# Performance work log

Hardware: AMD Instinct MI355X
Metric: run time of the kernel (lower is better)

Reference implementation:

```python
import jax, jax.numpy as jnp
import numpy as np

NUM_HEADS = 16
ROPE_SEGMENTS = (1024, 512)  # remainder of the sequence is left un-roped
ROPE_THETA = 10000.0
EPS = 1e-6


def _rmsnorm(t, w):
    # t: [B,H,N,D]; norm over last dim in fp32, then scale
    tf = t.astype(jnp.float32)
    n = tf * jax.lax.rsqrt(jnp.mean(tf * tf, axis=-1, keepdims=True) + EPS)
    return n.astype(t.dtype) * w


def _rope(t):
    # t: [B,H,S,D]; positions restart at 0 for each call (segment-local RoPE)
    S, D = t.shape[-2], t.shape[-1]
    inv_freq = 1.0 / (ROPE_THETA ** (jnp.arange(0, D, 2, dtype=jnp.float32) / D))  # [D/2]
    ang = jnp.arange(S, dtype=jnp.float32)[:, None] * inv_freq[None, :]            # [S,D/2]
    cos, sin = jnp.cos(ang), jnp.sin(ang)
    t1, t2 = t[..., : D // 2], t[..., D // 2 :]
    return jnp.concatenate([t1 * cos - t2 * sin, t2 * cos + t1 * sin], axis=-1).astype(t.dtype)


def _segmented_rope(t, N):
    parts, start = [], 0
    for seg in ROPE_SEGMENTS:
        parts.append(_rope(t[:, :, start : start + seg, :]))
        start += seg
    if start < N:
        parts.append(t[:, :, start:, :])
    return jnp.concatenate(parts, axis=2)


def setup_inputs() -> dict:
    key = jax.random.key(0)
    ks = jax.random.split(key, 5)
    B, N, C = 2, 2048, 1024
    D = C // NUM_HEADS
    s = 1.0 / np.sqrt(C)
    return {
        "x": jax.random.normal(ks[0], (B, N, C), jnp.float32),
        "qkv_w": jax.random.normal(ks[1], (3 * C, C), jnp.float32) * s,
        "qkv_b": jax.random.normal(ks[2], (3 * C,), jnp.float32) * 0.02,
        "qn_w": jnp.ones((D,), jnp.float32),
        "kn_w": jnp.ones((D,), jnp.float32),
        "proj_w": jax.random.normal(ks[3], (C, C), jnp.float32) * s,
        "proj_b": jax.random.normal(ks[4], (C,), jnp.float32) * 0.02,
    }


def reference(x, qkv_w, qkv_b, qn_w, kn_w, proj_w, proj_b):
    B, N, C = x.shape
    H = NUM_HEADS
    D = C // H
    qkv = (x @ qkv_w.T + qkv_b).reshape(B, N, 3, H, D)
    qkv = jnp.transpose(qkv, (2, 0, 3, 1, 4))  # [3,B,H,N,D]
    q, k, v = qkv[0], qkv[1], qkv[2]
    q = _rmsnorm(q, qn_w)
    k = _rmsnorm(k, kn_w)
    q = _segmented_rope(q, N)
    k = _segmented_rope(k, N)
    scale = 1.0 / np.sqrt(D)  # SDPA default scale
    scores = jnp.einsum("bhqd,bhkd->bhqk", q, k) * scale
    attn = jax.nn.softmax(scores, axis=-1)
    out = jnp.einsum("bhqk,bhkd->bhqd", attn, v)           # [B,H,N,D]
    out = jnp.transpose(out, (0, 2, 1, 3)).reshape(B, N, C)
    return out @ proj_w.T + proj_b
```

## Files before the change

kernel.cpp:

```cpp
#include <hip/hip_runtime.h>

typedef __attribute__((ext_vector_type(8))) short short8;
typedef __attribute__((ext_vector_type(4))) float f32x4;
typedef __attribute__((ext_vector_type(16))) float f32x16;

__device__ __forceinline__ float bf2f(unsigned short u) {
    union { unsigned int i; float f; } c; c.i = ((unsigned int)u) << 16; return c.f;
}
__device__ __forceinline__ unsigned short f2bf(float f) {
    union { float f; unsigned int i; } c; c.f = f;
    unsigned int u = c.i;
    return (unsigned short)((u + 0x7fffu + ((u >> 16) & 1u)) >> 16);
}

__device__ __forceinline__ void glds16(const void* g, void* l) {
    __builtin_amdgcn_global_load_lds(
        (const __attribute__((address_space(1))) unsigned int*)g,
        (__attribute__((address_space(3))) unsigned int*)l, 16, 0, 0);
}

union i4s8 { int4 i; short8 s; };

__global__ __launch_bounds__(256) void prep(
    const float* __restrict__ x, const float* __restrict__ qkv_w,
    const float* __restrict__ proj_w,
    const float* __restrict__ qn_w, const float* __restrict__ kn_w,
    unsigned short* __restrict__ xb, unsigned short* __restrict__ qwb,
    unsigned short* __restrict__ pwb, float* __restrict__ mb2)
{
    const int b = blockIdx.x, tid = threadIdx.x;
    const float* src; unsigned short* dst; int i;
    if (b < 4096)      { src = x;      dst = xb;  i = b * 256 + tid; }
    else if (b < 7168) { src = qkv_w;  dst = qwb; i = (b - 4096) * 256 + tid; }
    else if (b < 8192) { src = proj_w; dst = pwb; i = (b - 7168) * 256 + tid; }
    else {
        if (tid < 64) {
            float a = fabsf(qn_w[tid]), bb = fabsf(kn_w[tid]);
#pragma unroll
            for (int off = 32; off; off >>= 1) {
                a = fmaxf(a, __shfl_xor(a, off));
                bb = fmaxf(bb, __shfl_xor(bb, off));
            }
            if (tid == 0) *mb2 = 8.0f * a * bb * 1.4426950408889634f;
        }
        return;
    }
    float4 v = ((const float4*)src)[i];
    ushort4 o;
    o.x = f2bf(v.x); o.y = f2bf(v.y); o.z = f2bf(v.z); o.w = f2bf(v.w);
    ((ushort4*)dst)[i] = o;
}

__global__ __launch_bounds__(256) void gemm_qkv(
    const unsigned short* __restrict__ A,
    const unsigned short* __restrict__ W,
    const float* __restrict__ bias,
    const float* __restrict__ qn_w, const float* __restrict__ kn_w,
    unsigned short* __restrict__ qb, unsigned short* __restrict__ kb,
    unsigned short* __restrict__ vt)
{
    __shared__ unsigned short pool[128 * 136];
    const int tid = threadIdx.x;
    const int w = tid >> 6, l = tid & 63, quad = l >> 4, low = l & 15;
    const int m0 = blockIdx.y * 128, n0 = blockIdx.x * 128;
    const int wm = w >> 1, wn = w & 1;
    const int K = 1024;

    f32x4 acc[4][4];
#pragma unroll
    for (int i = 0; i < 4; i++)
#pragma unroll
        for (int j = 0; j < 4; j++) acc[i][j] = (f32x4){0.f, 0.f, 0.f, 0.f};

    const int r1 = tid >> 2, p1 = tid & 3;
    const int c1 = p1 ^ ((r1 >> 1) & 3);
    const int r2 = r1 + 64;
    const int c2 = p1 ^ ((r2 >> 1) & 3);
    const unsigned short* ga1 = A + (size_t)(m0 + r1) * K + c1 * 8;
    const unsigned short* ga2 = A + (size_t)(m0 + r2) * K + c2 * 8;
    const unsigned short* gw1 = W + (size_t)(n0 + r1) * K + c1 * 8;
    const unsigned short* gw2 = W + (size_t)(n0 + r2) * K + c2 * 8;
    char* lA = (char*)pool + (w << 10);
    char* lW = (char*)pool + 8192 + (w << 10);

    for (int k0 = 0; k0 < K; k0 += 32) {
        __syncthreads();
        glds16(ga1 + k0, lA);
        glds16(ga2 + k0, lA + 4096);
        glds16(gw1 + k0, lW);
        glds16(gw2 + k0, lW + 4096);
        __syncthreads();
        short8 af[4], wf[4];
#pragma unroll
        for (int i = 0; i < 4; i++) {
            const int ra = wm * 64 + i * 16 + low;
            af[i] = *(const short8*)&pool[ra * 32 + (quad ^ ((ra >> 1) & 3)) * 8];
            const int rw = wn * 64 + i * 16 + low;
            wf[i] = *(const short8*)&pool[4096 + rw * 32 + (quad ^ ((rw >> 1) & 3)) * 8];
        }
#pragma unroll
        for (int i = 0; i < 4; i++)
#pragma unroll
            for (int j = 0; j < 4; j++)
                acc[i][j] = __builtin_amdgcn_mfma_f32_16x16x32_bf16(
                    af[i], wf[j], acc[i][j], 0, 0, 0);
    }

    const int colbase = n0 + wn * 64;
    const int t3 = n0 >> 10;
    const int hh = (colbase & 1023) >> 6;

    if (t3 == 2) {
        __syncthreads();
#pragma unroll
        for (int i = 0; i < 4; i++)
#pragma unroll
            for (int j = 0; j < 4; j++) {
                const int c = wn * 64 + j * 16 + low;
                const float bv = bias[n0 + c];
#pragma unroll
                for (int reg = 0; reg < 4; reg++) {
                    const int r = wm * 64 + i * 16 + quad * 4 + reg;
                    pool[c * 136 + r] = f2bf(acc[i][j][reg] + bv);
                }
            }
        __syncthreads();
        const int b_ = m0 >> 11, nbase = m0 & 2047;
        const int rch = (tid & 15) * 8;
#pragma unroll
        for (int p = 0; p < 8; p++) {
            const int c = (tid >> 4) + p * 16;
            const int gc = n0 + c;
            const int h2 = (gc & 1023) >> 6, d = gc & 63;
            const short8 vv = *(const short8*)&pool[c * 136 + rch];
            *(short8*)(vt + ((size_t)((b_ * 16 + h2) * 64 + d)) * 2048 + nbase + rch) = vv;
        }
        return;
    }

    const float* nw = (t3 == 0) ? qn_w : kn_w;
    float wv4[4];
#pragma unroll
    for (int j = 0; j < 4; j++) wv4[j] = nw[j * 16 + low];
    const float c0 = -2.0f * 13.287712379549449f / 64.0f;
    const float invA = exp2f(c0 * (float)low);
    const float invB = exp2f(c0 * (float)(16 + low));
    unsigned short* dqk = (t3 == 0) ? qb : kb;

#pragma unroll
    for (int i = 0; i < 4; i++) {
#pragma unroll
        for (int reg = 0; reg < 4; reg++) {
            const int gm = m0 + wm * 64 + i * 16 + quad * 4 + reg;
            const int b_ = gm >> 11, npos = gm & 2047;
            float v[4];
#pragma unroll
            for (int j = 0; j < 4; j++)
                v[j] = acc[i][j][reg] + bias[colbase + j * 16 + low];
            float ss = v[0]*v[0] + v[1]*v[1] + v[2]*v[2] + v[3]*v[3];
            ss += __shfl_xor(ss, 1); ss += __shfl_xor(ss, 2);
            ss += __shfl_xor(ss, 4); ss += __shfl_xor(ss, 8);
            const float r = rsqrtf(ss * (1.0f / 64.0f) + 1e-6f);
            float nv[4];
#pragma unroll
            for (int j = 0; j < 4; j++) nv[j] = v[j] * r * wv4[j];
            float o0, o1, o2, o3;
            if (npos < 1536) {
                const float p = (float)((npos < 1024) ? npos : (npos - 1024));
                float sA, cA, sB, cB;
                __sincosf(p * invA, &sA, &cA);
                __sincosf(p * invB, &sB, &cB);
                o0 = nv[0] * cA - nv[2] * sA;
                o1 = nv[1] * cB - nv[3] * sB;
                o2 = nv[2] * cA + nv[0] * sA;
                o3 = nv[3] * cB + nv[1] * sB;
            } else { o0 = nv[0]; o1 = nv[1]; o2 = nv[2]; o3 = nv[3]; }
            unsigned short* drow =
                dqk + ((size_t)(b_ * 16 + hh) * 2048 + npos) * 64 + low;
            drow[0]  = f2bf(o0);
            drow[16] = f2bf(o1);
            drow[32] = f2bf(o2);
            drow[48] = f2bf(o3);
        }
    }
}

__global__ __launch_bounds__(256, 4) void flash_mfma(
    const unsigned short* __restrict__ qg, const unsigned short* __restrict__ kg,
    const unsigned short* __restrict__ vg, unsigned short* __restrict__ po,
    float* __restrict__ pl, const float* __restrict__ mb2p)
{
    __shared__ unsigned short Ks[128 * 64];
    __shared__ unsigned short Vs[64 * 128];

    const int tid = threadIdx.x;
    const int w = tid >> 6, lane = tid & 63, h5 = lane >> 5, l5 = lane & 31;
    const int bh = blockIdx.y, q0 = blockIdx.x * 128, half = blockIdx.z;
    const float MB2 = *mb2p;
    const float SCL = 0.125f * 1.4426950408889634f;

    short8 qf[4];
    {
        const unsigned short* qrow = qg + ((size_t)bh * 2048 + q0 + w * 32 + l5) * 64;
#pragma unroll
        for (int ks = 0; ks < 4; ks++)
            qf[ks] = *(const short8*)(qrow + ks * 16 + h5 * 8);
    }

    f32x16 o0, o1, ls;
#pragma unroll
    for (int i = 0; i < 16; i++) { o0[i] = 0.f; o1[i] = 0.f; ls[i] = 0.f; }
    i4s8 ones; ones.i = make_int4(0x3F803F80, 0x3F803F80, 0x3F803F80, 0x3F803F80);

    const int krr = tid >> 3, kc = (tid & 7) ^ (krr & 7);
    const unsigned short* gk = kg + ((size_t)bh * 2048 + krr) * 64 + kc * 8;
    const int vrr = tid >> 4, vc = (tid & 15) ^ (vrr & 15);
    const unsigned short* gv = vg + ((size_t)bh * 64 + vrr) * 2048 + vc * 8;
    char* lK = (char*)Ks + (w << 10);
    char* lV = (char*)Vs + (w << 10);
    const int kbase = half * 1024;

    for (int kt = 0; kt < 8; kt++) {
        const size_t ko = (size_t)(kbase + kt * 128);
        __syncthreads();
        glds16(gk + ko * 64,         lK);
        glds16(gk + ko * 64 + 2048,  lK + 4096);
        glds16(gk + ko * 64 + 4096,  lK + 8192);
        glds16(gk + ko * 64 + 6144,  lK + 12288);
        glds16(gv + ko,              lV);
        glds16(gv + ko + 32768,      lV + 4096);
        glds16(gv + ko + 65536,      lV + 8192);
        glds16(gv + ko + 98304,      lV + 12288);
        __syncthreads();

#pragma unroll
        for (int kbk = 0; kbk < 4; kbk++) {
            f32x16 s;
#pragma unroll
            for (int i = 0; i < 16; i++) s[i] = 0.f;
            const int krow = kbk * 32 + l5;
#pragma unroll
            for (int ks = 0; ks < 4; ks++) {
                const int ch = (h5 + 2 * ks) ^ (krow & 7);
                const short8 kf = *(const short8*)&Ks[krow * 64 + ch * 8];
                s = __builtin_amdgcn_mfma_f32_32x32x16_bf16(kf, qf[ks], s, 0, 0, 0);
            }
            unsigned int dw[8], pdw[8];
#pragma unroll
            for (int r = 0; r < 8; r++) {
                union { float f; unsigned int u; } a, b;
                a.f = exp2f(fmaf(s[2 * r],     SCL, -MB2));
                b.f = exp2f(fmaf(s[2 * r + 1], SCL, -MB2));
                dw[r] = __builtin_amdgcn_perm(b.u, a.u, 0x07060302u);
            }
#pragma unroll
            for (int r = 0; r < 8; r++) pdw[r] = __shfl_xor((int)dw[r], 32);
            i4s8 f0, f1;
            f0.i.x = h5 ? pdw[2] : dw[0];
            f0.i.y = h5 ? pdw[3] : dw[1];
            f0.i.z = h5 ? dw[2]  : pdw[0];
            f0.i.w = h5 ? dw[3]  : pdw[1];
            f1.i.x = h5 ? pdw[6] : dw[4];
            f1.i.y = h5 ? pdw[7] : dw[5];
            f1.i.z = h5 ? dw[6]  : pdw[4];
            f1.i.w = h5 ? dw[7]  : pdw[5];

            ls = __builtin_amdgcn_mfma_f32_32x32x16_bf16(f0.s, ones.s, ls, 0, 0, 0);
            ls = __builtin_amdgcn_mfma_f32_32x32x16_bf16(f1.s, ones.s, ls, 0, 0, 0);

#pragma unroll
            for (int nb = 0; nb < 2; nb++) {
                const int vrow = nb * 32 + l5;
                const int chb = kbk * 4 + h5;
                const short8 vfa = *(const short8*)&Vs[vrow * 128 + ((chb    ) ^ (vrow & 15)) * 8];
                const short8 vfb = *(const short8*)&Vs[vrow * 128 + ((chb + 2) ^ (vrow & 15)) * 8];
                f32x16& oo = nb ? o1 : o0;
                oo = __builtin_amdgcn_mfma_f32_32x32x16_bf16(f0.s, vfa, oo, 0, 0, 0);
                oo = __builtin_amdgcn_mfma_f32_32x32x16_bf16(f1.s, vfb, oo, 0, 0, 0);
            }
        }
    }

    unsigned short* pob = po + ((size_t)(half * 32 + bh)) * 2048 * 64;
    float* plb = pl + ((size_t)(half * 32 + bh)) * 2048;
#pragma unroll
    for (int r = 0; r < 16; r++) {
        const int qrow = q0 + w * 32 + (r & 3) + 8 * (r >> 2) + 4 * h5;
        pob[(size_t)qrow * 64 + l5]      = f2bf(o0[r]);
        pob[(size_t)qrow * 64 + 32 + l5] = f2bf(o1[r]);
        if (l5 == 0) plb[qrow] = ls[r];
    }
}

__global__ __launch_bounds__(256) void combine(
    const unsigned short* __restrict__ po, const float* __restrict__ pl,
    unsigned short* __restrict__ ao)
{
    const int g = blockIdx.x * 256 + threadIdx.x;
    const int row = g >> 3;
    const int c8 = (g & 7) * 8;
    const int bh = row >> 11, n = row & 2047;
    const float inv = 1.0f / (pl[row] + pl[65536 + row]);
    const short8 a = *(const short8*)(po + (size_t)row * 64 + c8);
    const short8 b = *(const short8*)(po + 4194304 + (size_t)row * 64 + c8);
    short8 r;
#pragma unroll
    for (int j = 0; j < 8; j++)
        r[j] = (short)f2bf((bf2f((unsigned short)a[j]) + bf2f((unsigned short)b[j])) * inv);
    const int b_ = bh >> 4, h = bh & 15;
    *(short8*)(ao + ((size_t)(b_ * 2048 + n)) * 1024 + h * 64 + c8) = r;
}

__global__ __launch_bounds__(256) void gemm_out(
    const unsigned short* __restrict__ A,
    const unsigned short* __restrict__ W,
    const float* __restrict__ bias,
    float* __restrict__ outp)
{
    __shared__ unsigned short As[64 * 32];
    __shared__ unsigned short Ws[128 * 32];
    const int tid = threadIdx.x;
    const int w = tid >> 6, l = tid & 63, quad = l >> 4, low = l & 15;
    const int m0 = blockIdx.y * 64, n0 = blockIdx.x * 128;
    const int wm = w >> 1, wn = w & 1;
    const int K = 1024;

    f32x4 acc[2][4];
#pragma unroll
    for (int i = 0; i < 2; i++)
#pragma unroll
        for (int j = 0; j < 4; j++) acc[i][j] = (f32x4){0.f, 0.f, 0.f, 0.f};

    const int r1 = tid >> 2, p1 = tid & 3;
    const int c1 = p1 ^ ((r1 >> 1) & 3);
    const int r2 = r1 + 64;
    const int c2 = p1 ^ ((r2 >> 1) & 3);
    const unsigned short* ga = A + (size_t)(m0 + r1) * K + c1 * 8;
    const unsigned short* gw1 = W + (size_t)(n0 + r1) * K + c1 * 8;
    const unsigned short* gw2 = W + (size_t)(n0 + r2) * K + c2 * 8;
    char* lA = (char*)As + (w << 10);
    char* lW = (char*)Ws + (w << 10);

    for (int k0 = 0; k0 < K; k0 += 32) {
        __syncthreads();
        glds16(ga + k0, lA);
        glds16(gw1 + k0, lW);
        glds16(gw2 + k0, lW + 4096);
        __syncthreads();
        short8 af[2], wf[4];
#pragma unroll
        for (int i = 0; i < 2; i++) {
            const int ra = wm * 32 + i * 16 + low;
            af[i] = *(const short8*)&As[ra * 32 + (quad ^ ((ra >> 1) & 3)) * 8];
        }
#pragma unroll
        for (int j = 0; j < 4; j++) {
            const int rw = wn * 64 + j * 16 + low;
            wf[j] = *(const short8*)&Ws[rw * 32 + (quad ^ ((rw >> 1) & 3)) * 8];
        }
#pragma unroll
        for (int i = 0; i < 2; i++)
#pragma unroll
            for (int j = 0; j < 4; j++)
                acc[i][j] = __builtin_amdgcn_mfma_f32_16x16x32_bf16(
                    af[i], wf[j], acc[i][j], 0, 0, 0);
    }

#pragma unroll
    for (int i = 0; i < 2; i++)
#pragma unroll
        for (int j = 0; j < 4; j++) {
            const int gc = n0 + wn * 64 + j * 16 + low;
            const float bv = bias[gc];
#pragma unroll
            for (int reg = 0; reg < 4; reg++) {
                const int gm = m0 + wm * 32 + i * 16 + quad * 4 + reg;
                outp[(size_t)gm * 1024 + gc] = acc[i][j][reg] + bv;
            }
        }
}

extern "C" void kernel_launch(void* const* d_in, const int* in_sizes, int n_in,
                              void* d_out, int out_size, void* d_ws, size_t ws_size,
                              hipStream_t stream)
{
    const float* x      = (const float*)d_in[0];
    const float* qkv_w  = (const float*)d_in[1];
    const float* qkv_b  = (const float*)d_in[2];
    const float* qn_w   = (const float*)d_in[3];
    const float* kn_w   = (const float*)d_in[4];
    const float* proj_w = (const float*)d_in[5];
    const float* proj_b = (const float*)d_in[6];

    char* base = (char*)d_ws;
    float* mb2          = (float*)base;
    unsigned short* pwb = (unsigned short*)(base + 256);
    unsigned short* qb  = pwb + 1048576;
    unsigned short* kb  = qb  + 4194304;
    unsigned short* vt  = kb  + 4194304;
    unsigned short* ao  = vt  + 4194304;
    unsigned short* xb  = ao  + 4194304;
    unsigned short* qwb = xb  + 4194304;
    unsigned short* po  = xb;
    float* pl           = (float*)(po + 8388608);

    prep<<<8193, 256, 0, stream>>>(x, qkv_w, proj_w, qn_w, kn_w, xb, qwb, pwb, mb2);

    gemm_qkv<<<dim3(24, 32), 256, 0, stream>>>(xb, qwb, qkv_b, qn_w, kn_w,
                                               qb, kb, vt);

    flash_mfma<<<dim3(16, 32, 2), 256, 0, stream>>>(qb, kb, vt, po, pl, mb2);

    combine<<<2048, 256, 0, stream>>>(po, pl, ao);

    gemm_out<<<dim3(8, 64), 256, 0, stream>>>(ao, pwb, proj_b, (float*)d_out);
}
```

Baseline: 216.7 us.

## Deepen GEMM K-tiles, shrink flash blocks, fold softmax scale into Q norm

Both GEMMs now stage 64-wide K slices per iteration, with an 8-way XOR swizzle and two MFMA sub-steps, which halves the number of barrier round-trips. The flash kernel switches to 128-thread blocks covering 64 queries with 64-key tiles, which doubles the grid and halves LDS per block. The softmax scale (1/sqrt(D)·log2e) is folded into the Q RMSNorm weight. The precomputed max-bound subtraction is dropped, along with the prep block that computed it, so exp2 is applied to raw scores. That removes an FMA per score and a kernel branch, but overflow safety now relies on the norm weights being small.

```diff
diff --git a/kernel.cpp b/kernel.cpp
--- a/kernel.cpp
+++ b/kernel.cpp
@@ -21,30 +21,19 @@
 
 union i4s8 { int4 i; short8 s; };
 
+#define SCL_F 0.18033688011112042f
+
 __global__ __launch_bounds__(256) void prep(
     const float* __restrict__ x, const float* __restrict__ qkv_w,
     const float* __restrict__ proj_w,
-    const float* __restrict__ qn_w, const float* __restrict__ kn_w,
     unsigned short* __restrict__ xb, unsigned short* __restrict__ qwb,
-    unsigned short* __restrict__ pwb, float* __restrict__ mb2)
+    unsigned short* __restrict__ pwb)
 {
     const int b = blockIdx.x, tid = threadIdx.x;
     const float* src; unsigned short* dst; int i;
     if (b < 4096)      { src = x;      dst = xb;  i = b * 256 + tid; }
     else if (b < 7168) { src = qkv_w;  dst = qwb; i = (b - 4096) * 256 + tid; }
-    else if (b < 8192) { src = proj_w; dst = pwb; i = (b - 7168) * 256 + tid; }
-    else {
-        if (tid < 64) {
-            float a = fabsf(qn_w[tid]), bb = fabsf(kn_w[tid]);
-#pragma unroll
-            for (int off = 32; off; off >>= 1) {
-                a = fmaxf(a, __shfl_xor(a, off));
-                bb = fmaxf(bb, __shfl_xor(bb, off));
-            }
-            if (tid == 0) *mb2 = 8.0f * a * bb * 1.4426950408889634f;
-        }
-        return;
-    }
+    else               { src = proj_w; dst = pwb; i = (b - 7168) * 256 + tid; }
     float4 v = ((const float4*)src)[i];
     ushort4 o;
     o.x = f2bf(v.x); o.y = f2bf(v.y); o.z = f2bf(v.z); o.w = f2bf(v.w);
@@ -72,38 +61,40 @@
 #pragma unroll
         for (int j = 0; j < 4; j++) acc[i][j] = (f32x4){0.f, 0.f, 0.f, 0.f};
 
-    const int r1 = tid >> 2, p1 = tid & 3;
-    const int c1 = p1 ^ ((r1 >> 1) & 3);
-    const int r2 = r1 + 64;
-    const int c2 = p1 ^ ((r2 >> 1) & 3);
-    const unsigned short* ga1 = A + (size_t)(m0 + r1) * K + c1 * 8;
-    const unsigned short* ga2 = A + (size_t)(m0 + r2) * K + c2 * 8;
-    const unsigned short* gw1 = W + (size_t)(n0 + r1) * K + c1 * 8;
-    const unsigned short* gw2 = W + (size_t)(n0 + r2) * K + c2 * 8;
+    const int r1 = tid >> 3, p1 = tid & 7, c1 = p1 ^ (r1 & 7);
+    const unsigned short* ga = A + (size_t)(m0 + r1) * K + c1 * 8;
+    const unsigned short* gw = W + (size_t)(n0 + r1) * K + c1 * 8;
     char* lA = (char*)pool + (w << 10);
-    char* lW = (char*)pool + 8192 + (w << 10);
-
-    for (int k0 = 0; k0 < K; k0 += 32) {
-        __syncthreads();
-        glds16(ga1 + k0, lA);
-        glds16(ga2 + k0, lA + 4096);
-        glds16(gw1 + k0, lW);
-        glds16(gw2 + k0, lW + 4096);
-        __syncthreads();
-        short8 af[4], wf[4];
-#pragma unroll
-        for (int i = 0; i < 4; i++) {
-            const int ra = wm * 64 + i * 16 + low;
-            af[i] = *(const short8*)&pool[ra * 32 + (quad ^ ((ra >> 1) & 3)) * 8];
-            const int rw = wn * 64 + i * 16 + low;
-            wf[i] = *(const short8*)&pool[4096 + rw * 32 + (quad ^ ((rw >> 1) & 3)) * 8];
-        }
-#pragma unroll
-        for (int i = 0; i < 4; i++)
-#pragma unroll
-            for (int j = 0; j < 4; j++)
-                acc[i][j] = __builtin_amdgcn_mfma_f32_16x16x32_bf16(
-                    af[i], wf[j], acc[i][j], 0, 0, 0);
+    char* lW = (char*)pool + 16384 + (w << 10);
+
+    for (int k0 = 0; k0 < K; k0 += 64) {
+        __syncthreads();
+        glds16(ga + k0,            lA);
+        glds16(ga + k0 + 32 * K,   lA + 4096);
+        glds16(ga + k0 + 64 * K,   lA + 8192);
+        glds16(ga + k0 + 96 * K,   lA + 12288);
+        glds16(gw + k0,            lW);
+        glds16(gw + k0 + 32 * K,   lW + 4096);
+        glds16(gw + k0 + 64 * K,   lW + 8192);
+        glds16(gw + k0 + 96 * K,   lW + 12288);
+        __syncthreads();
+#pragma unroll
+        for (int ks = 0; ks < 2; ks++) {
+            short8 af[4], wf[4];
+#pragma unroll
+            for (int i = 0; i < 4; i++) {
+                const int ra = wm * 64 + i * 16 + low;
+                af[i] = *(const short8*)&pool[ra * 64 + ((ks * 4 + quad) ^ (ra & 7)) * 8];
+                const int rw = wn * 64 + i * 16 + low;
+                wf[i] = *(const short8*)&pool[8192 + rw * 64 + ((ks * 4 + quad) ^ (rw & 7)) * 8];
+            }
+#pragma unroll
+            for (int i = 0; i < 4; i++)
+#pragma unroll
+                for (int j = 0; j < 4; j++)
+                    acc[i][j] = __builtin_amdgcn_mfma_f32_16x16x32_bf16(
+                        af[i], wf[j], acc[i][j], 0, 0, 0);
+        }
     }
 
     const int colbase = n0 + wn * 64;
@@ -139,9 +130,10 @@
     }
 
     const float* nw = (t3 == 0) ? qn_w : kn_w;
+    const float wscl = (t3 == 0) ? SCL_F : 1.0f;
     float wv4[4];
 #pragma unroll
-    for (int j = 0; j < 4; j++) wv4[j] = nw[j * 16 + low];
+    for (int j = 0; j < 4; j++) wv4[j] = nw[j * 16 + low] * wscl;
     const float c0 = -2.0f * 13.287712379549449f / 64.0f;
     const float invA = exp2f(c0 * (float)low);
     const float invB = exp2f(c0 * (float)(16 + low));
@@ -185,19 +177,17 @@
     }
 }
 
-__global__ __launch_bounds__(256, 4) void flash_mfma(
+__global__ __launch_bounds__(128, 4) void flash_mfma(
     const unsigned short* __restrict__ qg, const unsigned short* __restrict__ kg,
     const unsigned short* __restrict__ vg, unsigned short* __restrict__ po,
-    float* __restrict__ pl, const float* __restrict__ mb2p)
-{
-    __shared__ unsigned short Ks[128 * 64];
-    __shared__ unsigned short Vs[64 * 128];
+    float* __restrict__ pl)
+{
+    __shared__ unsigned short Ks[64 * 64];
+    __shared__ unsigned short Vs[64 * 64];
 
     const int tid = threadIdx.x;
     const int w = tid >> 6, lane = tid & 63, h5 = lane >> 5, l5 = lane & 31;
-    const int bh = blockIdx.y, q0 = blockIdx.x * 128, half = blockIdx.z;
-    const float MB2 = *mb2p;
-    const float SCL = 0.125f * 1.4426950408889634f;
+    const int bh = blockIdx.y, q0 = blockIdx.x * 64, half = blockIdx.z;
 
     short8 qf[4];
     {
@@ -212,29 +202,28 @@
     for (int i = 0; i < 16; i++) { o0[i] = 0.f; o1[i] = 0.f; ls[i] = 0.f; }
     i4s8 ones; ones.i = make_int4(0x3F803F80, 0x3F803F80, 0x3F803F80, 0x3F803F80);
 
-    const int krr = tid >> 3, kc = (tid & 7) ^ (krr & 7);
-    const unsigned short* gk = kg + ((size_t)bh * 2048 + krr) * 64 + kc * 8;
-    const int vrr = tid >> 4, vc = (tid & 15) ^ (vrr & 15);
-    const unsigned short* gv = vg + ((size_t)bh * 64 + vrr) * 2048 + vc * 8;
+    const int rr = tid >> 3, cc = (tid & 7) ^ (rr & 7);
+    const unsigned short* gk = kg + ((size_t)bh * 2048 + rr) * 64 + cc * 8;
+    const unsigned short* gv = vg + ((size_t)bh * 64 + rr) * 2048 + cc * 8;
     char* lK = (char*)Ks + (w << 10);
     char* lV = (char*)Vs + (w << 10);
     const int kbase = half * 1024;
 
-    for (int kt = 0; kt < 8; kt++) {
-        const size_t ko = (size_t)(kbase + kt * 128);
-        __syncthreads();
-        glds16(gk + ko * 64,         lK);
-        glds16(gk + ko * 64 + 2048,  lK + 4096);
-        glds16(gk + ko * 64 + 4096,  lK + 8192);
-        glds16(gk + ko * 64 + 6144,  lK + 12288);
-        glds16(gv + ko,              lV);
-        glds16(gv + ko + 32768,      lV + 4096);
-        glds16(gv + ko + 65536,      lV + 8192);
-        glds16(gv + ko + 98304,      lV + 12288);
-        __syncthreads();
-
-#pragma unroll
-        for (int kbk = 0; kbk < 4; kbk++) {
+    for (int kt = 0; kt < 16; kt++) {
+        const size_t ko = (size_t)(kbase + kt * 64);
+        __syncthreads();
+        glds16(gk + ko * 64,          lK);
+        glds16(gk + ko * 64 + 1024,   lK + 2048);
+        glds16(gk + ko * 64 + 2048,   lK + 4096);
+        glds16(gk + ko * 64 + 3072,   lK + 6144);
+        glds16(gv + ko,               lV);
+        glds16(gv + ko + 32768,       lV + 2048);
+        glds16(gv + ko + 65536,       lV + 4096);
+        glds16(gv + ko + 98304,       lV + 6144);
+        __syncthreads();
+
+#pragma unroll
+        for (int kbk = 0; kbk < 2; kbk++) {
             f32x16 s;
 #pragma unroll
             for (int i = 0; i < 16; i++) s[i] = 0.f;
@@ -249,8 +238,8 @@
 #pragma unroll
             for (int r = 0; r < 8; r++) {
                 union { float f; unsigned int u; } a, b;
-                a.f = exp2f(fmaf(s[2 * r],     SCL, -MB2));
-                b.f = exp2f(fmaf(s[2 * r + 1], SCL, -MB2));
+                a.f = exp2f(s[2 * r]);
+                b.f = exp2f(s[2 * r + 1]);
                 dw[r] = __builtin_amdgcn_perm(b.u, a.u, 0x07060302u);
             }
 #pragma unroll
@@ -272,8 +261,8 @@
             for (int nb = 0; nb < 2; nb++) {
                 const int vrow = nb * 32 + l5;
                 const int chb = kbk * 4 + h5;
-                const short8 vfa = *(const short8*)&Vs[vrow * 128 + ((chb    ) ^ (vrow & 15)) * 8];
-                const short8 vfb = *(const short8*)&Vs[vrow * 128 + ((chb + 2) ^ (vrow & 15)) * 8];
+                const short8 vfa = *(const short8*)&Vs[vrow * 64 + ((chb    ) ^ (vrow & 7)) * 8];
+                const short8 vfb = *(const short8*)&Vs[vrow * 64 + ((chb + 2) ^ (vrow & 7)) * 8];
                 f32x16& oo = nb ? o1 : o0;
                 oo = __builtin_amdgcn_mfma_f32_32x32x16_bf16(f0.s, vfa, oo, 0, 0, 0);
                 oo = __builtin_amdgcn_mfma_f32_32x32x16_bf16(f1.s, vfb, oo, 0, 0, 0);
@@ -317,8 +306,8 @@
     const float* __restrict__ bias,
     float* __restrict__ outp)
 {
-    __shared__ unsigned short As[64 * 32];
-    __shared__ unsigned short Ws[128 * 32];
+    __shared__ unsigned short As[64 * 64];
+    __shared__ unsigned short Ws[128 * 64];
     const int tid = threadIdx.x;
     const int w = tid >> 6, l = tid & 63, quad = l >> 4, low = l & 15;
     const int m0 = blockIdx.y * 64, n0 = blockIdx.x * 128;
@@ -331,39 +320,41 @@
 #pragma unroll
         for (int j = 0; j < 4; j++) acc[i][j] = (f32x4){0.f, 0.f, 0.f, 0.f};
 
-    const int r1 = tid >> 2, p1 = tid & 3;
-    const int c1 = p1 ^ ((r1 >> 1) & 3);
-    const int r2 = r1 + 64;
-    const int c2 = p1 ^ ((r2 >> 1) & 3);
+    const int r1 = tid >> 3, p1 = tid & 7, c1 = p1 ^ (r1 & 7);
     const unsigned short* ga = A + (size_t)(m0 + r1) * K + c1 * 8;
-    const unsigned short* gw1 = W + (size_t)(n0 + r1) * K + c1 * 8;
-    const unsigned short* gw2 = W + (size_t)(n0 + r2) * K + c2 * 8;
+    const unsigned short* gw = W + (size_t)(n0 + r1) * K + c1 * 8;
     char* lA = (char*)As + (w << 10);
     char* lW = (char*)Ws + (w << 10);
 
-    for (int k0 = 0; k0 < K; k0 += 32) {
-        __syncthreads();
-        glds16(ga + k0, lA);
-        glds16(gw1 + k0, lW);
-        glds16(gw2 + k0, lW + 4096);
-        __syncthreads();
-        short8 af[2], wf[4];
-#pragma unroll
-        for (int i = 0; i < 2; i++) {
-            const int ra = wm * 32 + i * 16 + low;
-            af[i] = *(const short8*)&As[ra * 32 + (quad ^ ((ra >> 1) & 3)) * 8];
-        }
-#pragma unroll
-        for (int j = 0; j < 4; j++) {
-            const int rw = wn * 64 + j * 16 + low;
-            wf[j] = *(const short8*)&Ws[rw * 32 + (quad ^ ((rw >> 1) & 3)) * 8];
-        }
-#pragma unroll
-        for (int i = 0; i < 2; i++)
-#pragma unroll
-            for (int j = 0; j < 4; j++)
-                acc[i][j] = __builtin_amdgcn_mfma_f32_16x16x32_bf16(
-                    af[i], wf[j], acc[i][j], 0, 0, 0);
+    for (int k0 = 0; k0 < K; k0 += 64) {
+        __syncthreads();
+        glds16(ga + k0,           lA);
+        glds16(ga + k0 + 32 * K,  lA + 4096);
+        glds16(gw + k0,           lW);
+        glds16(gw + k0 + 32 * K,  lW + 4096);
+        glds16(gw + k0 + 64 * K,  lW + 8192);
+        glds16(gw + k0 + 96 * K,  lW + 12288);
+        __syncthreads();
+#pragma unroll
+        for (int ks = 0; ks < 2; ks++) {
+            short8 af[2], wf[4];
+#pragma unroll
+            for (int i = 0; i < 2; i++) {
+                const int ra = wm * 32 + i * 16 + low;
+                af[i] = *(const short8*)&As[ra * 64 + ((ks * 4 + quad) ^ (ra & 7)) * 8];
+            }
+#pragma unroll
+            for (int j = 0; j < 4; j++) {
+                const int rw = wn * 64 + j * 16 + low;
+                wf[j] = *(const short8*)&Ws[rw * 64 + ((ks * 4 + quad) ^ (rw & 7)) * 8];
+            }
+#pragma unroll
+            for (int i = 0; i < 2; i++)
+#pragma unroll
+                for (int j = 0; j < 4; j++)
+                    acc[i][j] = __builtin_amdgcn_mfma_f32_16x16x32_bf16(
+                        af[i], wf[j], acc[i][j], 0, 0, 0);
+        }
     }
 
 #pragma unroll
@@ -393,7 +384,6 @@
     const float* proj_b = (const float*)d_in[6];
 
     char* base = (char*)d_ws;
-    float* mb2          = (float*)base;
     unsigned short* pwb = (unsigned short*)(base + 256);
     unsigned short* qb  = pwb + 1048576;
     unsigned short* kb  = qb  + 4194304;
@@ -404,12 +394,12 @@
     unsigned short* po  = xb;
     float* pl           = (float*)(po + 8388608);
 
-    prep<<<8193, 256, 0, stream>>>(x, qkv_w, proj_w, qn_w, kn_w, xb, qwb, pwb, mb2);
+    prep<<<8192, 256, 0, stream>>>(x, qkv_w, proj_w, xb, qwb, pwb);
 
     gemm_qkv<<<dim3(24, 32), 256, 0, stream>>>(xb, qwb, qkv_b, qn_w, kn_w,
                                                qb, kb, vt);
 
-    flash_mfma<<<dim3(16, 32, 2), 256, 0, stream>>>(qb, kb, vt, po, pl, mb2);
+    flash_mfma<<<dim3(32, 32, 2), 128, 0, stream>>>(qb, kb, vt, po, pl);
 
     combine<<<2048, 256, 0, stream>>>(po, pl, ao);
 
```

Measured after the change: 213.2 us. No clear change (-1.6%).
